# Optimization experiments

Measured on AMD Instinct MI355X. Metric: run time of the kernel, lower is better.

## Reference

```python
import jax, jax.numpy as jnp
import numpy as np

TARGET_DIM, DRUG_DIM, INT_DIM, HID = 1024, 128, 128, 32
LN_EPS = 1e-5  # torch nn.LayerNorm default (module's eps arg is unused for LN)


def _layernorm(x, g, b):
    mu = jnp.mean(x, axis=-1, keepdims=True)
    var = jnp.var(x, axis=-1, keepdims=True)
    return (x - mu) * jax.lax.rsqrt(var + LN_EPS) * g + b


def setup_inputs() -> dict:
    key = jax.random.key(0)
    ks = jax.random.split(key, 10)
    B, NR, NA = 4, 512, 64
    s_t = 1.0 / np.sqrt(TARGET_DIM)
    s_d = 1.0 / np.sqrt(DRUG_DIM)
    s_o = 1.0 / np.sqrt(HID * HID)
    return {
        "target_embedding": jax.random.normal(ks[0], (B, NR, TARGET_DIM), jnp.float32),
        "drug_embedding": jax.random.normal(ks[1], (B, NA, DRUG_DIM), jnp.float32),
        "target_mask": jnp.ones((B, NR), jnp.float32),
        "drug_mask": jnp.ones((B, NA), jnp.float32),
        "ln_t_g": jnp.ones((TARGET_DIM,), jnp.float32),
        "ln_t_b": jnp.zeros((TARGET_DIM,), jnp.float32),
        "ln_d_g": jnp.ones((DRUG_DIM,), jnp.float32),
        "ln_d_b": jnp.zeros((DRUG_DIM,), jnp.float32),
        "W_t": jax.random.uniform(ks[2], (HID, TARGET_DIM), jnp.float32, -s_t, s_t),
        "b_t": jax.random.uniform(ks[3], (HID,), jnp.float32, -s_t, s_t),
        "W_d": jax.random.uniform(ks[4], (HID, DRUG_DIM), jnp.float32, -s_d, s_d),
        "b_d": jax.random.uniform(ks[5], (HID,), jnp.float32, -s_d, s_d),
        "W_out": jax.random.uniform(ks[6], (INT_DIM, HID * HID), jnp.float32, -s_o, s_o),
        "b_out": jax.random.uniform(ks[7], (INT_DIM,), jnp.float32, -s_o, s_o),
    }


def reference(target_embedding, drug_embedding, target_mask, drug_mask,
              ln_t_g, ln_t_b, ln_d_g, ln_d_b, W_t, b_t, W_d, b_d, W_out, b_out):
    t = _layernorm(target_embedding, ln_t_g, ln_t_b)
    d = _layernorm(drug_embedding, ln_d_g, ln_d_b)
    # projections + mask: [B,NR,H], [B,NA,H]
    tf = (t @ W_t.T + b_t) * target_mask[..., None]
    df = (d @ W_d.T + b_d) * drug_mask[..., None]
    # fused outer-product + linear_out: W_out row index i over flat (c*H+e)
    W3 = W_out.reshape(INT_DIM, HID, HID)  # [i, c, e]
    outer = jnp.einsum('bnc,bme,ice->bnmi', tf, df, W3) + b_out
    mask = target_mask[:, :, None] * drug_mask[:, None, :]  # [B,NR,NA]
    outer = outer * mask[..., None]
    return outer, mask
```

## Files before the change

kernel.cpp:

```cpp
#include <hip/hip_runtime.h>

typedef __attribute__((ext_vector_type(8))) short short8;
typedef __attribute__((ext_vector_type(4))) float f32x4;

#define LNP_YSTRIDE 1032

__device__ __forceinline__ unsigned short f2bf(float f) {
  union { float f; unsigned u; } v; v.f = f;
  unsigned r = v.u + 0x7FFFu + ((v.u >> 16) & 1u);
  return (unsigned short)(r >> 16);
}
__device__ __forceinline__ unsigned pack2(float a, float b) {
  return (unsigned)f2bf(a) | ((unsigned)f2bf(b) << 16);
}
__device__ __forceinline__ short8 packW(float4 a, float4 b) {
  union { short8 s; unsigned u[4]; } r;
  r.u[0] = pack2(a.x, a.y); r.u[1] = pack2(a.z, a.w);
  r.u[2] = pack2(b.x, b.y); r.u[3] = pack2(b.z, b.w);
  return r.s;
}

__device__ __forceinline__ void lnproj8_t(
    const float* __restrict__ X, const float* __restrict__ g, const float* __restrict__ bia,
    const float* __restrict__ W, const float* __restrict__ pb, const float* __restrict__ msk,
    unsigned short* __restrict__ outb, int row0, unsigned short* Yl, float* pd, int tid)
{
  const int w = tid >> 6, lid = tid & 63, l = tid & 15, q = (tid >> 4) & 3;
  const f32x4 zero = {0.f, 0.f, 0.f, 0.f};

  #pragma unroll
  for (int rr = 0; rr < 2; ++rr) {
    const int row = w * 2 + rr;
    const float* xr = X + (size_t)(row0 + row) * 1024;
    float4 v[4];
    float s = 0.f, s2 = 0.f;
    #pragma unroll
    for (int k = 0; k < 4; ++k) {
      v[k] = *(const float4*)(xr + 4 * lid + 256 * k);
      s  += (v[k].x + v[k].y) + (v[k].z + v[k].w);
      s2 += (v[k].x * v[k].x + v[k].y * v[k].y) + (v[k].z * v[k].z + v[k].w * v[k].w);
    }
    #pragma unroll
    for (int off = 32; off >= 1; off >>= 1) { s += __shfl_xor(s, off, 64); s2 += __shfl_xor(s2, off, 64); }
    const float mu = s * (1.f / 1024.f);
    const float rs = rsqrtf(s2 * (1.f / 1024.f) - mu * mu + 1e-5f);
    #pragma unroll
    for (int k = 0; k < 4; ++k) {
      float4 gg = *(const float4*)(g + 4 * lid + 256 * k);
      float4 bb = *(const float4*)(bia + 4 * lid + 256 * k);
      unsigned* yd = (unsigned*)(Yl + row * LNP_YSTRIDE + 4 * lid + 256 * k);
      yd[0] = pack2((v[k].x - mu) * rs * gg.x + bb.x, (v[k].y - mu) * rs * gg.y + bb.y);
      yd[1] = pack2((v[k].z - mu) * rs * gg.z + bb.z, (v[k].w - mu) * rs * gg.w + bb.w);
    }
  }
  __syncthreads();

  f32x4 acc0 = zero, acc1 = zero;
  #pragma unroll
  for (int ss = 0; ss < 8; ++ss) {
    const int s = w * 8 + ss;
    short8 af = *(const short8*)(Yl + l * LNP_YSTRIDE + s * 32 + q * 8);
    const float* wp0 = W + (size_t)l * 1024 + s * 32 + q * 8;
    const float* wp1 = W + (size_t)(16 + l) * 1024 + s * 32 + q * 8;
    acc0 = __builtin_amdgcn_mfma_f32_16x16x32_bf16(af, packW(*(const float4*)wp0, *(const float4*)(wp0 + 4)), acc0, 0, 0, 0);
    acc1 = __builtin_amdgcn_mfma_f32_16x16x32_bf16(af, packW(*(const float4*)wp1, *(const float4*)(wp1 + 4)), acc1, 0, 0, 0);
  }
  if (w > 0 && q < 2) {
    #pragma unroll
    for (int r = 0; r < 4; ++r) {
      const int rl = q * 4 + r;
      pd[(w - 1) * 256 + rl * 16 + l]       = acc0[r];
      pd[(w - 1) * 256 + 128 + rl * 16 + l] = acc1[r];
    }
  }
  __syncthreads();
  if (w == 0 && q < 2) {
    #pragma unroll
    for (int ht = 0; ht < 2; ++ht) {
      const int h = ht * 16 + l;
      const float pbv = pb[h];
      #pragma unroll
      for (int r = 0; r < 4; ++r) {
        const int rl = q * 4 + r, rg = row0 + rl;
        float val = (ht ? acc1[r] : acc0[r]) + pbv;
        #pragma unroll
        for (int k = 0; k < 3; ++k) val += pd[k * 256 + ht * 128 + rl * 16 + l];
        outb[(size_t)rg * 32 + h] = f2bf(val * msk[rg]);
      }
    }
  }
}

template<int ROWLEN>
__device__ __forceinline__ void lnproj(
    const float* __restrict__ X, const float* __restrict__ g, const float* __restrict__ bia,
    const float* __restrict__ W, const float* __restrict__ pb, const float* __restrict__ msk,
    unsigned short* __restrict__ outb, int row0, unsigned short* Yl, float* pd, int tid)
{
  const int w = tid >> 6, lid = tid & 63, l = tid & 15, q = (tid >> 4) & 3;

  #pragma unroll
  for (int rr = 0; rr < 4; ++rr) {
    const int row = w * 4 + rr;
    const float* xr = X + (size_t)(row0 + row) * ROWLEN;
    float2 v = *(const float2*)(xr + 2 * lid);
    float s = v.x + v.y, s2 = v.x * v.x + v.y * v.y;
    #pragma unroll
    for (int off = 32; off >= 1; off >>= 1) { s += __shfl_xor(s, off, 64); s2 += __shfl_xor(s2, off, 64); }
    const float mu = s * (1.f / ROWLEN);
    const float rs = rsqrtf(s2 * (1.f / ROWLEN) - mu * mu + 1e-5f);
    float2 gg = *(const float2*)(g + 2 * lid);
    float2 bb = *(const float2*)(bia + 2 * lid);
    *(unsigned*)(Yl + row * LNP_YSTRIDE + 2 * lid) =
        pack2((v.x - mu) * rs * gg.x + bb.x, (v.y - mu) * rs * gg.y + bb.y);
  }
  __syncthreads();

  const int KST = ROWLEN / 32;
  const int ht = w & 1, kh = w >> 1;
  const int h = ht * 16 + l;
  f32x4 acc = {0.f, 0.f, 0.f, 0.f};
  #pragma unroll
  for (int s = kh * (KST / 2); s < kh * (KST / 2) + KST / 2; ++s) {
    short8 af = *(const short8*)(Yl + l * LNP_YSTRIDE + s * 32 + q * 8);
    const float* wp = W + (size_t)h * ROWLEN + s * 32 + q * 8;
    short8 bf = packW(*(const float4*)wp, *(const float4*)(wp + 4));
    acc = __builtin_amdgcn_mfma_f32_16x16x32_bf16(af, bf, acc, 0, 0, 0);
  }
  if (w >= 2) {
    #pragma unroll
    for (int r = 0; r < 4; ++r) pd[ht * 256 + (q * 4 + r) * 16 + l] = acc[r];
  }
  __syncthreads();
  if (w < 2) {
    const float pbv = pb[h];
    #pragma unroll
    for (int r = 0; r < 4; ++r) {
      const int rg = row0 + q * 4 + r;
      float val = acc[r] + pd[ht * 256 + (q * 4 + r) * 16 + l] + pbv;
      val *= msk[rg];
      outb[(size_t)rg * 32 + h] = f2bf(val);
    }
  }
}

__global__ __launch_bounds__(256) void k_pre(
    const float* __restrict__ tgt, const float* __restrict__ drg,
    const float* __restrict__ tmask, const float* __restrict__ dmask,
    const float* __restrict__ ln_t_g, const float* __restrict__ ln_t_b,
    const float* __restrict__ ln_d_g, const float* __restrict__ ln_d_b,
    const float* __restrict__ W_t, const float* __restrict__ b_t,
    const float* __restrict__ W_d, const float* __restrict__ b_d,
    unsigned short* __restrict__ tfb, unsigned short* __restrict__ dfb,
    float* __restrict__ mask_out)
{
  __shared__ unsigned short Yl[16 * LNP_YSTRIDE];
  __shared__ float pd[3 * 256];
  const int blk = blockIdx.x, tid = threadIdx.x;
  if (blk < 256) {
    lnproj8_t(tgt, ln_t_g, ln_t_b, W_t, b_t, tmask, tfb, blk * 8, Yl, pd, tid);
  } else if (blk < 272) {
    lnproj<128>(drg, ln_d_g, ln_d_b, W_d, b_d, dmask, dfb, (blk - 256) * 16, Yl, pd, tid);
  } else {
    const int base = ((blk - 272) * 256 + tid) * 4;
    const int b = base >> 15;
    const float tm = tmask[base >> 6];
    float4 d = *(const float4*)(dmask + b * 64 + (base & 63));
    float4 o; o.x = tm * d.x; o.y = tm * d.y; o.z = tm * d.z; o.w = tm * d.w;
    *(float4*)(mask_out + base) = o;
  }
}

__global__ __launch_bounds__(256) void k_mid(
    const float* __restrict__ W_out, const unsigned short* __restrict__ dfb,
    unsigned short* __restrict__ Hb)
{
  const int id = blockIdx.x;
  const int b = id >> 6, icg = id & 63;
  const int tid = threadIdx.x, w = tid >> 6, l = tid & 15, q = (tid >> 4) & 3;
  const f32x4 zero = {0.f, 0.f, 0.f, 0.f};
  const int m = w * 16 + l;
  short8 bf = *(const short8*)(dfb + (size_t)(b * 64 + m) * 32 + q * 8);
  #pragma unroll
  for (int u = 0; u < 4; ++u) {
    const int ic0 = icg * 64 + u * 16;
    const float* ap = W_out + (size_t)(ic0 + l) * 32 + q * 8;
    short8 af = packW(*(const float4*)ap, *(const float4*)(ap + 4));
    f32x4 d = __builtin_amdgcn_mfma_f32_16x16x32_bf16(af, bf, zero, 0, 0, 0);
    uint2 hv; hv.x = pack2(d[0], d[1]); hv.y = pack2(d[2], d[3]);
    *(uint2*)(Hb + (size_t)(b * 64 + m) * 4096 + ic0 + q * 4) = hv;
  }
}

__global__ __launch_bounds__(256) void k_main(
    const unsigned short* __restrict__ Hb, const unsigned short* __restrict__ tfb,
    const float* __restrict__ b_out, const float* __restrict__ tmask,
    const float* __restrict__ dmask, float* __restrict__ out)
{
  const int id = blockIdx.x;
  const int b = id >> 9, m = (id >> 3) & 63, ng = id & 7;
  const int tid = threadIdx.x, w = tid >> 6, l = tid & 15, q = (tid >> 4) & 3;
  const int n0 = ng * 64;
  const f32x4 zero = {0.f, 0.f, 0.f, 0.f};

  const unsigned short* hrow = Hb + (size_t)(b * 64 + m) * 4096;
  short8 a0 = *(const short8*)(hrow + (w * 32 + l) * 32 + q * 8);
  short8 a1 = *(const short8*)(hrow + (w * 32 + 16 + l) * 32 + q * 8);

  short8 bfr[4];
  #pragma unroll
  for (int t2 = 0; t2 < 4; ++t2)
    bfr[t2] = *(const short8*)(tfb + (size_t)(b * 512 + n0 + t2 * 16 + l) * 32 + q * 8);

  const float4 bo0 = *(const float4*)(b_out + w * 32 + q * 4);
  const float4 bo1 = *(const float4*)(b_out + w * 32 + 16 + q * 4);
  const float dmv = dmask[b * 64 + m];
  float tmv[4];
  #pragma unroll
  for (int t2 = 0; t2 < 4; ++t2)
    tmv[t2] = tmask[b * 512 + n0 + t2 * 16 + l] * dmv;

  #pragma unroll
  for (int t2 = 0; t2 < 4; ++t2) {
    const size_t rbase = ((size_t)(b * 512 + n0 + t2 * 16 + l) * 64 + m) * 128;
    const float s = tmv[t2];
    f32x4 d0 = __builtin_amdgcn_mfma_f32_16x16x32_bf16(a0, bfr[t2], zero, 0, 0, 0);
    f32x4 d1 = __builtin_amdgcn_mfma_f32_16x16x32_bf16(a1, bfr[t2], zero, 0, 0, 0);
    f32x4 o0, o1;
    o0[0] = (d0[0] + bo0.x) * s; o0[1] = (d0[1] + bo0.y) * s;
    o0[2] = (d0[2] + bo0.z) * s; o0[3] = (d0[3] + bo0.w) * s;
    o1[0] = (d1[0] + bo1.x) * s; o1[1] = (d1[1] + bo1.y) * s;
    o1[2] = (d1[2] + bo1.z) * s; o1[3] = (d1[3] + bo1.w) * s;
    __builtin_nontemporal_store(o0, (f32x4*)(out + rbase + w * 32 + q * 4));
    __builtin_nontemporal_store(o1, (f32x4*)(out + rbase + w * 32 + 16 + q * 4));
  }
}

extern "C" void kernel_launch(void* const* d_in, const int* in_sizes, int n_in,
                              void* d_out, int out_size, void* d_ws, size_t ws_size,
                              hipStream_t stream)
{
  const float* tgt    = (const float*)d_in[0];
  const float* drg    = (const float*)d_in[1];
  const float* tmask  = (const float*)d_in[2];
  const float* dmask  = (const float*)d_in[3];
  const float* ln_t_g = (const float*)d_in[4];
  const float* ln_t_b = (const float*)d_in[5];
  const float* ln_d_g = (const float*)d_in[6];
  const float* ln_d_b = (const float*)d_in[7];
  const float* W_t    = (const float*)d_in[8];
  const float* b_t    = (const float*)d_in[9];
  const float* W_d    = (const float*)d_in[10];
  const float* b_d    = (const float*)d_in[11];
  const float* W_out  = (const float*)d_in[12];
  const float* b_out  = (const float*)d_in[13];

  float* out = (float*)d_out;
  float* mask_out = out + (size_t)4 * 512 * 64 * 128;

  char* ws = (char*)d_ws;
  unsigned short* Hb  = (unsigned short*)(ws);
  unsigned short* tfb = (unsigned short*)(ws + 2097152);
  unsigned short* dfb = (unsigned short*)(ws + 2097152 + 131072);

  k_pre<<<dim3(400), dim3(256), 0, stream>>>(
      tgt, drg, tmask, dmask, ln_t_g, ln_t_b, ln_d_g, ln_d_b,
      W_t, b_t, W_d, b_d, tfb, dfb, mask_out);
  k_mid<<<dim3(256), dim3(256), 0, stream>>>(W_out, dfb, Hb);
  k_main<<<dim3(2048), dim3(256), 0, stream>>>(Hb, tfb, b_out, tmask, dmask, out);
}
```

Measured before the change: 122.9 us.

## Fuse drug LN/projection into H computation and drop separate mid kernel

Removes the k_mid launch by having 256 k_pre blocks each recompute the drug LayerNorm and W_d projection for their batch and build the H tile directly. Wave shuffles rearrange the projection output into the B-fragment layout for the W_out MFMA. This saves one kernel launch and the dfb round trip, but repeats the drug LN/projection 64 times per batch. It also swaps the nontemporal output stores in k_main for plain stores.

```diff
diff --git a/kernel.cpp b/kernel.cpp
--- a/kernel.cpp
+++ b/kernel.cpp
@@ -4,6 +4,7 @@
 typedef __attribute__((ext_vector_type(4))) float f32x4;
 
 #define LNP_YSTRIDE 1032
+#define DYSTR 136
 
 __device__ __forceinline__ unsigned short f2bf(float f) {
   union { float f; unsigned u; } v; v.f = f;
@@ -91,56 +92,70 @@
   }
 }
 
-template<int ROWLEN>
-__device__ __forceinline__ void lnproj(
-    const float* __restrict__ X, const float* __restrict__ g, const float* __restrict__ bia,
-    const float* __restrict__ W, const float* __restrict__ pb, const float* __restrict__ msk,
-    unsigned short* __restrict__ outb, int row0, unsigned short* Yl, float* pd, int tid)
+__device__ __forceinline__ void drug_h(
+    const float* __restrict__ drg, const float* __restrict__ g, const float* __restrict__ bia,
+    const float* __restrict__ W_d, const float* __restrict__ b_d, const float* __restrict__ dmask,
+    const float* __restrict__ W_out, unsigned short* __restrict__ Hb,
+    int b, int icg, unsigned short* Yl, int tid)
 {
   const int w = tid >> 6, lid = tid & 63, l = tid & 15, q = (tid >> 4) & 3;
-
-  #pragma unroll
-  for (int rr = 0; rr < 4; ++rr) {
-    const int row = w * 4 + rr;
-    const float* xr = X + (size_t)(row0 + row) * ROWLEN;
+  const f32x4 zero = {0.f, 0.f, 0.f, 0.f};
+
+  #pragma unroll
+  for (int rr = 0; rr < 16; ++rr) {
+    const int row = w * 16 + rr;
+    const float* xr = drg + (size_t)(b * 64 + row) * 128;
     float2 v = *(const float2*)(xr + 2 * lid);
     float s = v.x + v.y, s2 = v.x * v.x + v.y * v.y;
     #pragma unroll
     for (int off = 32; off >= 1; off >>= 1) { s += __shfl_xor(s, off, 64); s2 += __shfl_xor(s2, off, 64); }
-    const float mu = s * (1.f / ROWLEN);
-    const float rs = rsqrtf(s2 * (1.f / ROWLEN) - mu * mu + 1e-5f);
+    const float mu = s * (1.f / 128.f);
+    const float rs = rsqrtf(s2 * (1.f / 128.f) - mu * mu + 1e-5f);
     float2 gg = *(const float2*)(g + 2 * lid);
     float2 bb = *(const float2*)(bia + 2 * lid);
-    *(unsigned*)(Yl + row * LNP_YSTRIDE + 2 * lid) =
+    *(unsigned*)(Yl + row * DYSTR + 2 * lid) =
         pack2((v.x - mu) * rs * gg.x + bb.x, (v.y - mu) * rs * gg.y + bb.y);
   }
-  __syncthreads();
-
-  const int KST = ROWLEN / 32;
-  const int ht = w & 1, kh = w >> 1;
-  const int h = ht * 16 + l;
-  f32x4 acc = {0.f, 0.f, 0.f, 0.f};
-  #pragma unroll
-  for (int s = kh * (KST / 2); s < kh * (KST / 2) + KST / 2; ++s) {
-    short8 af = *(const short8*)(Yl + l * LNP_YSTRIDE + s * 32 + q * 8);
-    const float* wp = W + (size_t)h * ROWLEN + s * 32 + q * 8;
-    short8 bf = packW(*(const float4*)wp, *(const float4*)(wp + 4));
-    acc = __builtin_amdgcn_mfma_f32_16x16x32_bf16(af, bf, acc, 0, 0, 0);
-  }
-  if (w >= 2) {
-    #pragma unroll
-    for (int r = 0; r < 4; ++r) pd[ht * 256 + (q * 4 + r) * 16 + l] = acc[r];
-  }
-  __syncthreads();
-  if (w < 2) {
-    const float pbv = pb[h];
-    #pragma unroll
-    for (int r = 0; r < 4; ++r) {
-      const int rg = row0 + q * 4 + r;
-      float val = acc[r] + pd[ht * 256 + (q * 4 + r) * 16 + l] + pbv;
-      val *= msk[rg];
-      outb[(size_t)rg * 32 + h] = f2bf(val);
-    }
+
+  f32x4 acc0 = zero, acc1 = zero;
+  #pragma unroll
+  for (int s = 0; s < 4; ++s) {
+    short8 bf = *(const short8*)(Yl + (w * 16 + l) * DYSTR + s * 32 + q * 8);
+    const float* wp0 = W_d + (size_t)l * 128 + s * 32 + q * 8;
+    const float* wp1 = W_d + (size_t)(16 + l) * 128 + s * 32 + q * 8;
+    acc0 = __builtin_amdgcn_mfma_f32_16x16x32_bf16(packW(*(const float4*)wp0, *(const float4*)(wp0 + 4)), bf, acc0, 0, 0, 0);
+    acc1 = __builtin_amdgcn_mfma_f32_16x16x32_bf16(packW(*(const float4*)wp1, *(const float4*)(wp1 + 4)), bf, acc1, 0, 0, 0);
+  }
+  const float dmv = dmask[b * 64 + w * 16 + l];
+  const float4 bd0 = *(const float4*)(b_d + q * 4);
+  const float4 bd1 = *(const float4*)(b_d + 16 + q * 4);
+  unsigned u0a = pack2((acc0[0] + bd0.x) * dmv, (acc0[1] + bd0.y) * dmv);
+  unsigned u0b = pack2((acc0[2] + bd0.z) * dmv, (acc0[3] + bd0.w) * dmv);
+  unsigned u1a = pack2((acc1[0] + bd1.x) * dmv, (acc1[1] + bd1.y) * dmv);
+  unsigned u1b = pack2((acc1[2] + bd1.z) * dmv, (acc1[3] + bd1.w) * dmv);
+
+  const int srcA = ((q & 1) << 5) + l;
+  const int srcB = srcA + 16;
+  unsigned a0 = __shfl((int)u0a, srcA, 64), a1 = __shfl((int)u1a, srcA, 64);
+  unsigned b0 = __shfl((int)u0b, srcA, 64), b1 = __shfl((int)u1b, srcA, 64);
+  unsigned c0 = __shfl((int)u0a, srcB, 64), c1 = __shfl((int)u1a, srcB, 64);
+  unsigned d0 = __shfl((int)u0b, srcB, 64), d1 = __shfl((int)u1b, srcB, 64);
+  const bool hi = (q >= 2);
+  union { short8 s; unsigned u[4]; } bfrag;
+  bfrag.u[0] = hi ? a1 : a0;
+  bfrag.u[1] = hi ? b1 : b0;
+  bfrag.u[2] = hi ? c1 : c0;
+  bfrag.u[3] = hi ? d1 : d0;
+
+  const int m = w * 16 + l;
+  #pragma unroll
+  for (int u = 0; u < 4; ++u) {
+    const int ic0 = icg * 64 + u * 16;
+    const float* ap = W_out + (size_t)(ic0 + l) * 32 + q * 8;
+    short8 af = packW(*(const float4*)ap, *(const float4*)(ap + 4));
+    f32x4 d = __builtin_amdgcn_mfma_f32_16x16x32_bf16(af, bfrag.s, zero, 0, 0, 0);
+    uint2 hv; hv.x = pack2(d[0], d[1]); hv.y = pack2(d[2], d[3]);
+    *(uint2*)(Hb + (size_t)(b * 64 + m) * 4096 + ic0 + q * 4) = hv;
   }
 }
 
@@ -151,7 +166,8 @@
     const float* __restrict__ ln_d_g, const float* __restrict__ ln_d_b,
     const float* __restrict__ W_t, const float* __restrict__ b_t,
     const float* __restrict__ W_d, const float* __restrict__ b_d,
-    unsigned short* __restrict__ tfb, unsigned short* __restrict__ dfb,
+    const float* __restrict__ W_out,
+    unsigned short* __restrict__ tfb, unsigned short* __restrict__ Hb,
     float* __restrict__ mask_out)
 {
   __shared__ unsigned short Yl[16 * LNP_YSTRIDE];
@@ -159,36 +175,16 @@
   const int blk = blockIdx.x, tid = threadIdx.x;
   if (blk < 256) {
     lnproj8_t(tgt, ln_t_g, ln_t_b, W_t, b_t, tmask, tfb, blk * 8, Yl, pd, tid);
-  } else if (blk < 272) {
-    lnproj<128>(drg, ln_d_g, ln_d_b, W_d, b_d, dmask, dfb, (blk - 256) * 16, Yl, pd, tid);
+  } else if (blk < 512) {
+    drug_h(drg, ln_d_g, ln_d_b, W_d, b_d, dmask, W_out, Hb,
+           (blk - 256) >> 6, (blk - 256) & 63, Yl, tid);
   } else {
-    const int base = ((blk - 272) * 256 + tid) * 4;
+    const int base = ((blk - 512) * 256 + tid) * 4;
     const int b = base >> 15;
     const float tm = tmask[base >> 6];
     float4 d = *(const float4*)(dmask + b * 64 + (base & 63));
     float4 o; o.x = tm * d.x; o.y = tm * d.y; o.z = tm * d.z; o.w = tm * d.w;
     *(float4*)(mask_out + base) = o;
-  }
-}
-
-__global__ __launch_bounds__(256) void k_mid(
-    const float* __restrict__ W_out, const unsigned short* __restrict__ dfb,
-    unsigned short* __restrict__ Hb)
-{
-  const int id = blockIdx.x;
-  const int b = id >> 6, icg = id & 63;
-  const int tid = threadIdx.x, w = tid >> 6, l = tid & 15, q = (tid >> 4) & 3;
-  const f32x4 zero = {0.f, 0.f, 0.f, 0.f};
-  const int m = w * 16 + l;
-  short8 bf = *(const short8*)(dfb + (size_t)(b * 64 + m) * 32 + q * 8);
-  #pragma unroll
-  for (int u = 0; u < 4; ++u) {
-    const int ic0 = icg * 64 + u * 16;
-    const float* ap = W_out + (size_t)(ic0 + l) * 32 + q * 8;
-    short8 af = packW(*(const float4*)ap, *(const float4*)(ap + 4));
-    f32x4 d = __builtin_amdgcn_mfma_f32_16x16x32_bf16(af, bf, zero, 0, 0, 0);
-    uint2 hv; hv.x = pack2(d[0], d[1]); hv.y = pack2(d[2], d[3]);
-    *(uint2*)(Hb + (size_t)(b * 64 + m) * 4096 + ic0 + q * 4) = hv;
   }
 }
 
@@ -231,8 +227,8 @@
     o0[2] = (d0[2] + bo0.z) * s; o0[3] = (d0[3] + bo0.w) * s;
     o1[0] = (d1[0] + bo1.x) * s; o1[1] = (d1[1] + bo1.y) * s;
     o1[2] = (d1[2] + bo1.z) * s; o1[3] = (d1[3] + bo1.w) * s;
-    __builtin_nontemporal_store(o0, (f32x4*)(out + rbase + w * 32 + q * 4));
-    __builtin_nontemporal_store(o1, (f32x4*)(out + rbase + w * 32 + 16 + q * 4));
+    *(f32x4*)(out + rbase + w * 32 + q * 4) = o0;
+    *(f32x4*)(out + rbase + w * 32 + 16 + q * 4) = o1;
   }
 }
 
@@ -261,11 +257,9 @@
   char* ws = (char*)d_ws;
   unsigned short* Hb  = (unsigned short*)(ws);
   unsigned short* tfb = (unsigned short*)(ws + 2097152);
-  unsigned short* dfb = (unsigned short*)(ws + 2097152 + 131072);
-
-  k_pre<<<dim3(400), dim3(256), 0, stream>>>(
+
+  k_pre<<<dim3(640), dim3(256), 0, stream>>>(
       tgt, drg, tmask, dmask, ln_t_g, ln_t_b, ln_d_g, ln_d_b,
-      W_t, b_t, W_d, b_d, tfb, dfb, mask_out);
-  k_mid<<<dim3(256), dim3(256), 0, stream>>>(W_out, dfb, Hb);
+      W_t, b_t, W_d, b_d, W_out, tfb, Hb, mask_out);
   k_main<<<dim3(2048), dim3(256), 0, stream>>>(Hb, tfb, b_out, tmask, dmask, out);
 }
```

New measurement: 119.1 us. 3.1% less time.
